# Kernel optimization log

Hardware: AMD Instinct MI355X
Metric: run time of the kernel (lower is better)

The kernel has to match this reference:

```python
import jax, jax.numpy as jnp
import numpy as np

B, H, T, D = 2, 16, 2048, 64
BASE_WINDOW = 256
FULL = 999999


def _make_window_sizes(num_heads=H, base_window=BASE_WINDOW):
    ws = []
    for h in range(num_heads):
        if h < num_heads // 4:
            ws.append(base_window)
        elif h < num_heads // 2:
            ws.append(base_window * 2)
        elif h < 3 * num_heads // 4:
            ws.append(base_window * 4)
        else:
            ws.append(FULL)
    return jnp.asarray(ws, dtype=jnp.int32)


def setup_inputs() -> dict:
    key = jax.random.key(0)
    kq, kk, kv = jax.random.split(key, 3)
    Q = jax.random.normal(kq, (B, H, T, D), dtype=jnp.float32)
    K = jax.random.normal(kk, (B, H, T, D), dtype=jnp.float32)
    V = jax.random.normal(kv, (B, H, T, D), dtype=jnp.float32)
    return {"Q": Q, "K": K, "V": V, "window_sizes": _make_window_sizes()}


def reference(Q, K, V, window_sizes):
    b, h, t, d = Q.shape
    scale = 1.0 / np.sqrt(d).astype(np.float32)
    idx = jnp.arange(t, dtype=jnp.int32)
    diff = idx[:, None] - idx[None, :]  # [T, T], q_idx - kv_idx
    # causal & |q-k| <= w  ==  0 <= diff <= w  (per head)
    mask = (diff >= 0) & (diff[None, :, :] <= window_sizes[:, None, None])  # [H, T, T]
    scores = jnp.einsum('bhqd,bhkd->bhqk', Q, K) * scale  # [B, H, T, T]
    scores = jnp.where(mask[None], scores, -jnp.inf)
    attn = jax.nn.softmax(scores, axis=-1)
    return jnp.einsum('bhqk,bhkd->bhqd', attn, V)
```

## Files before the change

### kernel.cpp

```cpp
#include <hip/hip_runtime.h>
#include <hip/hip_bf16.h>


constexpr int Bc = 2, Hc = 16, Tc = 2048, Dc = 64;
constexpr int BQ = 64;
constexpr int BK = 32;
constexpr float QSCALE = 0.125f * 1.44269504088896340736f;
constexpr float CMAX = 16.0f;

constexpr size_t KB_OFF = 256;
constexpr size_t VB_OFF = 256 + (size_t)Bc * Hc * Tc * Dc * 2;
constexpr int HEADE = Tc * Dc;

constexpr int KOFF = 0;
constexpr int VOFF = 8192;
constexpr int POFF = 18432;

typedef __attribute__((ext_vector_type(8))) short short8;
typedef __attribute__((ext_vector_type(4))) float float4v;

#if defined(__has_builtin)
#if __has_builtin(__builtin_amdgcn_exp2f)
#define EXP2 __builtin_amdgcn_exp2f
#endif
#endif
#ifndef EXP2
#define EXP2 exp2f
#endif

__device__ inline unsigned f2bf_u(float f) {
    union { float f; unsigned u; } v; v.f = f;
    return (v.u + 0x7fffu + ((v.u >> 16) & 1u)) >> 16;
}

__device__ inline short8 pack8(const float* t) {
    short8 r;
#pragma unroll
    for (int j = 0; j < 8; j++) r[j] = (short)f2bf_u(t[j]);
    return r;
}

__device__ inline unsigned pk_bf16(float a, float b) {
    __hip_bfloat162 h = __float22bfloat162_rn(make_float2(a, b));
    union { __hip_bfloat162 h; unsigned u; } v; v.h = h;
    return v.u;
}

__global__ __launch_bounds__(256)
void preconv_kernel(const float* __restrict__ K, const float* __restrict__ V,
                    unsigned short* __restrict__ Kb, unsigned short* __restrict__ Vtb) {
    const int blk = blockIdx.x;
    const int tid = threadIdx.x;
    if (blk < 2048) {
        const int base = blk * 2048 + tid * 8;
        float4v a = *(const float4v*)(K + base);
        float4v b = *(const float4v*)(K + base + 4);
        float t[8] = {a[0], a[1], a[2], a[3], b[0], b[1], b[2], b[3]};
        *(short8*)(Kb + base) = pack8(t);
    } else {
        __shared__ float tile[64][65];
        const int blk2 = blk - 2048;
        const int bh = blk2 >> 5;
        const int t0 = (blk2 & 31) * 64;
        const float* src = V + (size_t)bh * HEADE + (size_t)t0 * Dc;
#pragma unroll
        for (int i = 0; i < 4; i++) {
            const int r = (tid >> 4) + i * 16;
            const int d4 = (tid & 15) * 4;
            float4v v4 = *(const float4v*)(src + r * Dc + d4);
            tile[r][d4] = v4[0]; tile[r][d4 + 1] = v4[1];
            tile[r][d4 + 2] = v4[2]; tile[r][d4 + 3] = v4[3];
        }
        __syncthreads();
        unsigned short* dst = Vtb + (size_t)bh * HEADE + t0;
#pragma unroll
        for (int i = 0; i < 2; i++) {
            const int d = (tid >> 3) + 32 * i;
            const int c = tid & 7;
            float t[8];
#pragma unroll
            for (int j = 0; j < 8; j++) t[j] = tile[c * 8 + j][d];
            *(short8*)(dst + (size_t)d * Tc + c * 8) = pack8(t);
        }
    }
}

__global__ __launch_bounds__(256, 4)
void dswa_kernel(const float* __restrict__ Q,
                 const unsigned short* __restrict__ Kb,
                 const unsigned short* __restrict__ Vtb,
                 const int* __restrict__ wsz,
                 float* __restrict__ O) {
    __shared__ __align__(16) unsigned short LDS[20480];

    const int tid  = threadIdx.x;
    const int wave = tid >> 6;
    const int g    = wave >> 1;
    const int wq   = wave & 1;
    const int lane = tid & 63;
    const int quad = lane >> 4;
    const int l16  = lane & 15;
    const int ksw  = 0;  (void)ksw;
    const int psw  = (l16 & 3) << 3;

    unsigned short* Kg = &LDS[KOFF + g * 4096];
    unsigned short* Vg = &LDS[VOFF + g * 5120];
    unsigned short* Pl = &LDS[POFF + wave * 512];

    const int l128 = tid & 127;
    const int krow = l128 >> 2;
    const int kcol = (l128 & 3) * 16;
    const int vrow = l128 >> 1;
    const int vcol = (l128 & 1) * 16;

    const int blk = blockIdx.x;
    const int b  = blk & 1;
    const int qt = 31 - ((blk >> 1) & 31);
    const int h  = 15 - (blk >> 6);
    const int q0 = qt * BQ;
    const int win = wsz[h];

    const size_t headoff = (size_t)(b * Hc + h) * HEADE;
    const float* Qp = Q + headoff;
    const unsigned short* Kbh = Kb + headoff;
    const unsigned short* Vbh = Vtb + headoff;
    float* Op = O + headoff;

    short8 qf[2][2];
#pragma unroll
    for (int s = 0; s < 2; s++) {
        const int qrow = q0 + wq * 32 + s * 16 + l16;
#pragma unroll
        for (int c = 0; c < 2; c++) {
            const float* src = Qp + (size_t)qrow * Dc + c * 32 + quad * 8;
            float4v a = *(const float4v*)src;
            float4v d4 = *(const float4v*)(src + 4);
            float t[8] = {a[0]*QSCALE, a[1]*QSCALE, a[2]*QSCALE, a[3]*QSCALE,
                          d4[0]*QSCALE, d4[1]*QSCALE, d4[2]*QSCALE, d4[3]*QSCALE};
            qf[s][c] = pack8(t);
        }
    }

    float4v acc[2][4];
#pragma unroll
    for (int s = 0; s < 2; s++)
#pragma unroll
        for (int nb = 0; nb < 4; nb++) acc[s][nb] = (float4v){0.f, 0.f, 0.f, 0.f};
    float lp0 = 0.0f, lp1 = 0.0f;

    const int kv_lo = (max(0, q0 - win)) & ~(BK - 1);
    const int n_tiles = (q0 + BQ - kv_lo) >> 5;
    const int IT = (n_tiles + 1) >> 1;

    const int kv0g = kv_lo + g * BK;
    const unsigned short* kgp = Kbh + (size_t)(kv0g + krow) * Dc + kcol;
    const unsigned short* vgp = Vbh + (size_t)vrow * Tc + kv0g + vcol;

    short8 kr0, kr1, vr0, vr1;
    if (g < n_tiles) {
        kr0 = *(const short8*)(kgp);
        kr1 = *(const short8*)(kgp + 8);
        vr0 = *(const short8*)(vgp);
        vr1 = *(const short8*)(vgp + 8);
    }
    kgp += 64 * Dc; vgp += 64;

    for (int t = 0; t < IT; ++t) {
        const int ti = g + 2 * t;
        const bool act = ti < n_tiles;
        const int kv0 = kv_lo + ti * BK;
        unsigned short* Kl = Kg + (t & 1) * 2048;
        unsigned short* Vt = Vg + (t & 1) * 2560;

        if (act) {
            const int ks = (krow & 7) << 3;
            *(short8*)&Kl[krow * 64 + (kcol ^ ks)] = kr0;
            *(short8*)&Kl[krow * 64 + ((kcol + 8) ^ ks)] = kr1;
            *(short8*)&Vt[vrow * 40 + vcol] = vr0;
            *(short8*)&Vt[vrow * 40 + vcol + 8] = vr1;
        }
        __syncthreads();

        if (ti + 2 < n_tiles) {
            kr0 = *(const short8*)(kgp);
            kr1 = *(const short8*)(kgp + 8);
            vr0 = *(const short8*)(vgp);
            vr1 = *(const short8*)(vgp + 8);
        }
        kgp += 64 * Dc; vgp += 64;

        if (act) {
            float4v sT0[2], sT1[2];
#pragma unroll
            for (int mb = 0; mb < 2; mb++) {
                float4v c0 = {-CMAX, -CMAX, -CMAX, -CMAX};
                float4v c1 = {-CMAX, -CMAX, -CMAX, -CMAX};
#pragma unroll
                for (int ch = 0; ch < 2; ch++) {
                    const int row = mb * 16 + l16;
                    short8 kf = *(short8*)&Kl[row * 64 +
                                              ((ch * 32 + quad * 8) ^ ((row & 7) << 3))];
                    c0 = __builtin_amdgcn_mfma_f32_16x16x32_bf16(kf, qf[0][ch], c0, 0, 0, 0);
                    c1 = __builtin_amdgcn_mfma_f32_16x16x32_bf16(kf, qf[1][ch], c1, 0, 0, 0);
                }
                sT0[mb] = c0; sT1[mb] = c1;
            }

            short8 pf0, pf1;
            {
                const int rs = q0 + wq * 32;
                const bool interior = (kv0 + 31 <= rs) && (rs + 15 - kv0 <= win);
                if (!interior) {
                    const int dbase = rs + l16 - kv0 - quad * 4;
#pragma unroll
                    for (int mb = 0; mb < 2; mb++)
#pragma unroll
                        for (int r = 0; r < 4; r++) {
                            const unsigned diff = (unsigned)(dbase - mb * 16 - r);
                            sT0[mb][r] = (diff <= (unsigned)win) ? sT0[mb][r] : -3.0e38f;
                        }
                }
#pragma unroll
                for (int mb = 0; mb < 2; mb++) {
                    float p0 = EXP2(sT0[mb][0]);
                    float p1 = EXP2(sT0[mb][1]);
                    float p2 = EXP2(sT0[mb][2]);
                    float p3 = EXP2(sT0[mb][3]);
                    lp0 += (p0 + p1) + (p2 + p3);
                    unsigned* dst = (unsigned*)&Pl[l16 * 32 + ((mb * 16 + quad * 4) ^ psw)];
                    dst[0] = pk_bf16(p0, p1);
                    dst[1] = pk_bf16(p2, p3);
                }
                __asm__ volatile("" ::: "memory");
                pf0 = *(short8*)&Pl[l16 * 32 + ((quad * 8) ^ psw)];
            }
            {
                const int rs = q0 + wq * 32 + 16;
                const bool interior = (kv0 + 31 <= rs) && (rs + 15 - kv0 <= win);
                if (!interior) {
                    const int dbase = rs + l16 - kv0 - quad * 4;
#pragma unroll
                    for (int mb = 0; mb < 2; mb++)
#pragma unroll
                        for (int r = 0; r < 4; r++) {
                            const unsigned diff = (unsigned)(dbase - mb * 16 - r);
                            sT1[mb][r] = (diff <= (unsigned)win) ? sT1[mb][r] : -3.0e38f;
                        }
                }
                __asm__ volatile("" ::: "memory");
#pragma unroll
                for (int mb = 0; mb < 2; mb++) {
                    float p0 = EXP2(sT1[mb][0]);
                    float p1 = EXP2(sT1[mb][1]);
                    float p2 = EXP2(sT1[mb][2]);
                    float p3 = EXP2(sT1[mb][3]);
                    lp1 += (p0 + p1) + (p2 + p3);
                    unsigned* dst = (unsigned*)&Pl[l16 * 32 + ((mb * 16 + quad * 4) ^ psw)];
                    dst[0] = pk_bf16(p0, p1);
                    dst[1] = pk_bf16(p2, p3);
                }
                __asm__ volatile("" ::: "memory");
                pf1 = *(short8*)&Pl[l16 * 32 + ((quad * 8) ^ psw)];
            }

#pragma unroll
            for (int nb = 0; nb < 4; nb++) {
                short8 vf = *(short8*)&Vt[(nb * 16 + l16) * 40 + quad * 8];
                acc[0][nb] = __builtin_amdgcn_mfma_f32_16x16x32_bf16(pf0, vf, acc[0][nb], 0, 0, 0);
                acc[1][nb] = __builtin_amdgcn_mfma_f32_16x16x32_bf16(pf1, vf, acc[1][nb], 0, 0, 0);
            }
        }
    }

    lp0 += __shfl_xor(lp0, 16); lp0 += __shfl_xor(lp0, 32);
    lp1 += __shfl_xor(lp1, 16); lp1 += __shfl_xor(lp1, 32);

    __syncthreads();
    float* fl = (float*)LDS;
    if (g == 1) {
#pragma unroll
        for (int s = 0; s < 2; s++) {
            if (quad == 0) fl[(wq * 32 + s * 16 + l16) * 66 + 64] = (s ? lp1 : lp0);
#pragma unroll
            for (int r = 0; r < 4; r++) {
                const int row = wq * 32 + s * 16 + quad * 4 + r;
#pragma unroll
                for (int nb = 0; nb < 4; nb++)
                    fl[row * 66 + nb * 16 + l16] = acc[s][nb][r];
            }
        }
    }
    __syncthreads();
    if (g == 0) {
#pragma unroll
        for (int s = 0; s < 2; s++) {
            const float lps = s ? lp1 : lp0;
#pragma unroll
            for (int r = 0; r < 4; r++) {
                const int row = wq * 32 + s * 16 + quad * 4 + r;
                const float l0 = __shfl(lps, quad * 4 + r);
                const float lt = l0 + fl[row * 66 + 64];
                const float inv = 1.0f / lt;
                float* dst = Op + (size_t)(q0 + row) * Dc;
#pragma unroll
                for (int nb = 0; nb < 4; nb++)
                    dst[nb * 16 + l16] = (acc[s][nb][r] + fl[row * 66 + nb * 16 + l16]) * inv;
            }
        }
    }
}

extern "C" void kernel_launch(void* const* d_in, const int* in_sizes, int n_in,
                              void* d_out, int out_size, void* d_ws, size_t ws_size,
                              hipStream_t stream) {
    (void)in_sizes; (void)n_in; (void)ws_size; (void)out_size;
    const float* Q = (const float*)d_in[0];
    const float* K = (const float*)d_in[1];
    const float* V = (const float*)d_in[2];
    const int* wsz = (const int*)d_in[3];
    float* Out = (float*)d_out;

    unsigned short* Kb  = (unsigned short*)((char*)d_ws + KB_OFF);
    unsigned short* Vtb = (unsigned short*)((char*)d_ws + VB_OFF);

    preconv_kernel<<<dim3(3072), dim3(256), 0, stream>>>(K, V, Kb, Vtb);
    dswa_kernel<<<dim3(1024), dim3(256), 0, stream>>>(Q, Kb, Vtb, wsz, Out);
}
```

Baseline: 125.8 us.

## Replace LDS round-trip for P fragments with permlane swaps and reorder block schedule

The softmax probability tile P is now rearranged from the MFMA accumulator layout into the A-operand layout with permlane32/permlane16 swap intrinsics in registers, instead of a write to and read back from LDS. This drops the per-wave P scratch area from LDS, shrinking the allocation, and removes LDS store/load latency and traffic from the inner loop. Block-to-work mapping also changes: heads are grouped by window class in slots, with alternating q-tile order, to even out load across CUs. The risk is that the cross-lane permutation does not reproduce the original fragment layout exactly.

```diff
diff --git a/kernel.cpp b/kernel.cpp
--- a/kernel.cpp
+++ b/kernel.cpp
@@ -14,10 +14,10 @@
 
 constexpr int KOFF = 0;
 constexpr int VOFF = 8192;
-constexpr int POFF = 18432;
 
 typedef __attribute__((ext_vector_type(8))) short short8;
 typedef __attribute__((ext_vector_type(4))) float float4v;
+typedef __attribute__((ext_vector_type(2))) unsigned int uint2v;
 
 #if defined(__has_builtin)
 #if __has_builtin(__builtin_amdgcn_exp2f)
@@ -44,6 +44,12 @@
     __hip_bfloat162 h = __float22bfloat162_rn(make_float2(a, b));
     union { __hip_bfloat162 h; unsigned u; } v; v.h = h;
     return v.u;
+}
+
+__device__ inline short8 mk8(unsigned a0, unsigned a1, unsigned a2, unsigned a3) {
+    union { unsigned u[4]; short8 s; } v;
+    v.u[0] = a0; v.u[1] = a1; v.u[2] = a2; v.u[3] = a3;
+    return v.s;
 }
 
 __global__ __launch_bounds__(256)
@@ -91,7 +97,7 @@
                  const unsigned short* __restrict__ Vtb,
                  const int* __restrict__ wsz,
                  float* __restrict__ O) {
-    __shared__ __align__(16) unsigned short LDS[20480];
+    __shared__ __align__(16) unsigned short LDS[18432];
 
     const int tid  = threadIdx.x;
     const int wave = tid >> 6;
@@ -100,12 +106,9 @@
     const int lane = tid & 63;
     const int quad = lane >> 4;
     const int l16  = lane & 15;
-    const int ksw  = 0;  (void)ksw;
-    const int psw  = (l16 & 3) << 3;
 
     unsigned short* Kg = &LDS[KOFF + g * 4096];
     unsigned short* Vg = &LDS[VOFF + g * 5120];
-    unsigned short* Pl = &LDS[POFF + wave * 512];
 
     const int l128 = tid & 127;
     const int krow = l128 >> 2;
@@ -113,12 +116,16 @@
     const int vrow = l128 >> 1;
     const int vcol = (l128 & 1) * 16;
 
-    const int blk = blockIdx.x;
-    const int b  = blk & 1;
-    const int qt = 31 - ((blk >> 1) & 31);
-    const int h  = 15 - (blk >> 6);
-    const int q0 = qt * BQ;
-    const int win = wsz[h];
+    const int blk  = blockIdx.x;
+    const int ci   = blk & 255;
+    const int slot = blk >> 8;
+    const int b    = ci & 1;
+    const int q5   = (ci >> 1) & 31;
+    const int hh   = ci >> 6;
+    const int h    = (3 - slot) * 4 + hh;
+    const int qt   = (slot == 0) ? q5 : 31 - q5;
+    const int q0   = qt * BQ;
+    const int win  = wsz[h];
 
     const size_t headoff = (size_t)(b * Hc + h) * HEADE;
     const float* Qp = Q + headoff;
@@ -220,6 +227,7 @@
                             sT0[mb][r] = (diff <= (unsigned)win) ? sT0[mb][r] : -3.0e38f;
                         }
                 }
+                unsigned w[4];
 #pragma unroll
                 for (int mb = 0; mb < 2; mb++) {
                     float p0 = EXP2(sT0[mb][0]);
@@ -227,12 +235,14 @@
                     float p2 = EXP2(sT0[mb][2]);
                     float p3 = EXP2(sT0[mb][3]);
                     lp0 += (p0 + p1) + (p2 + p3);
-                    unsigned* dst = (unsigned*)&Pl[l16 * 32 + ((mb * 16 + quad * 4) ^ psw)];
-                    dst[0] = pk_bf16(p0, p1);
-                    dst[1] = pk_bf16(p2, p3);
-                }
-                __asm__ volatile("" ::: "memory");
-                pf0 = *(short8*)&Pl[l16 * 32 + ((quad * 8) ^ psw)];
+                    w[2 * mb]     = pk_bf16(p0, p1);
+                    w[2 * mb + 1] = pk_bf16(p2, p3);
+                }
+                uint2v pa = __builtin_amdgcn_permlane32_swap(w[0], w[2], false, false);
+                uint2v c02 = __builtin_amdgcn_permlane16_swap(pa[0], pa[1], false, false);
+                uint2v pb = __builtin_amdgcn_permlane32_swap(w[1], w[3], false, false);
+                uint2v c13 = __builtin_amdgcn_permlane16_swap(pb[0], pb[1], false, false);
+                pf0 = mk8(c02[0], c13[0], c02[1], c13[1]);
             }
             {
                 const int rs = q0 + wq * 32 + 16;
@@ -247,7 +257,7 @@
                             sT1[mb][r] = (diff <= (unsigned)win) ? sT1[mb][r] : -3.0e38f;
                         }
                 }
-                __asm__ volatile("" ::: "memory");
+                unsigned w[4];
 #pragma unroll
                 for (int mb = 0; mb < 2; mb++) {
                     float p0 = EXP2(sT1[mb][0]);
@@ -255,12 +265,14 @@
                     float p2 = EXP2(sT1[mb][2]);
                     float p3 = EXP2(sT1[mb][3]);
                     lp1 += (p0 + p1) + (p2 + p3);
-                    unsigned* dst = (unsigned*)&Pl[l16 * 32 + ((mb * 16 + quad * 4) ^ psw)];
-                    dst[0] = pk_bf16(p0, p1);
-                    dst[1] = pk_bf16(p2, p3);
-                }
-                __asm__ volatile("" ::: "memory");
-                pf1 = *(short8*)&Pl[l16 * 32 + ((quad * 8) ^ psw)];
+                    w[2 * mb]     = pk_bf16(p0, p1);
+                    w[2 * mb + 1] = pk_bf16(p2, p3);
+                }
+                uint2v pa = __builtin_amdgcn_permlane32_swap(w[0], w[2], false, false);
+                uint2v c02 = __builtin_amdgcn_permlane16_swap(pa[0], pa[1], false, false);
+                uint2v pb = __builtin_amdgcn_permlane32_swap(w[1], w[3], false, false);
+                uint2v c13 = __builtin_amdgcn_permlane16_swap(pb[0], pb[1], false, false);
+                pf1 = mk8(c02[0], c13[0], c02[1], c13[1]);
             }
 
 #pragma unroll
```

After: 120.7 us. 4.0% less time.
